# Optimization experiments

Measured on AMD Instinct MI355X. Metric: run time of the kernel, lower is better.

Reference implementation:

```python
import jax, jax.numpy as jnp
import numpy as np

B, T, C = 2, 4096, 768
H = 12
D = C // H  # head_size = 64


def setup_inputs() -> dict:
    key = jax.random.key(0)
    k1, k2, k3 = jax.random.split(key, 3)
    x = jax.random.normal(k1, (B, T, C), dtype=jnp.float32)
    w_attn = jax.random.normal(k2, (C, 3 * C), dtype=jnp.float32) * (C ** -0.5)
    b_attn = jnp.zeros((3 * C,), dtype=jnp.float32)
    w_proj = jax.random.normal(k3, (C, C), dtype=jnp.float32) * (C ** -0.5)
    b_proj = jnp.zeros((C,), dtype=jnp.float32)
    return {"x": x, "w_attn": w_attn, "b_attn": b_attn, "w_proj": w_proj, "b_proj": b_proj}


def reference(x, w_attn, b_attn, w_proj, b_proj):
    Bx, Tx, Cx = x.shape
    # fused QKV projection
    qkv = x @ w_attn + b_attn  # (B, T, 3C)
    q, k, v = jnp.split(qkv, 3, axis=2)
    # (B, H, T, D)
    q = q.reshape(Bx, Tx, H, D).transpose(0, 2, 1, 3)
    k = k.reshape(Bx, Tx, H, D).transpose(0, 2, 1, 3)
    v = v.reshape(Bx, Tx, H, D).transpose(0, 2, 1, 3)
    scale = 1.0 / jnp.sqrt(jnp.asarray(D, dtype=x.dtype))
    scores = jnp.einsum('bhqd,bhkd->bhqk', q, k) * scale  # (B, H, T, T)
    causal = jnp.tril(jnp.ones((Tx, Tx), dtype=bool))
    scores = jnp.where(causal, scores, jnp.asarray(-jnp.inf, dtype=scores.dtype))
    attn = jax.nn.softmax(scores, axis=-1)
    y = jnp.einsum('bhqk,bhkd->bhqd', attn, v)  # (B, H, T, D)
    y = y.transpose(0, 2, 1, 3).reshape(Bx, Tx, Cx)
    return y @ w_proj + b_proj
```

## Files before the change

### kernel.cpp

```cpp
#include <hip/hip_runtime.h>
#include <stdint.h>

#define B_   2
#define T_   4096
#define C_   768
#define H_   12
#define D_   64
#define BH_  24
#define M_   8192
#define K_   768
#define N1_  2304

#define NEG_BIG (-1.0e30f)
#define QSCALE 0.18033688011112042f

typedef short bf16x8 __attribute__((ext_vector_type(8)));
typedef float f32x4  __attribute__((ext_vector_type(4)));
typedef float f32x16 __attribute__((ext_vector_type(16)));
typedef uint32_t u32x4 __attribute__((ext_vector_type(4)));
typedef int i32x2 __attribute__((ext_vector_type(2)));

typedef const __attribute__((address_space(1))) void* as1cv;
typedef __attribute__((address_space(3))) void*       as3v;

__device__ __forceinline__ void gload_lds16(const void* g, void* l) {
  __builtin_amdgcn_global_load_lds((as1cv)g, (as3v)l, 16, 0, 0);
}

__device__ __forceinline__ unsigned short f2bf(float f) {
  uint32_t x = __builtin_bit_cast(uint32_t, f);
  uint32_t r = (x + 0x7fffu + ((x >> 16) & 1u)) >> 16;
  return (unsigned short)r;
}

__device__ __forceinline__ unsigned short f2bf_hu(float f) {
  return (unsigned short)((__builtin_bit_cast(uint32_t, f) + 0x8000u) >> 16);
}

#if __has_builtin(__builtin_amdgcn_perm)
__device__ __forceinline__ uint32_t pack_hu(float lo, float hi) {
  uint32_t a = __builtin_bit_cast(uint32_t, lo) + 0x8000u;
  uint32_t b = __builtin_bit_cast(uint32_t, hi) + 0x8000u;
  return __builtin_amdgcn_perm(b, a, 0x07060302u);
}
#else
__device__ __forceinline__ uint32_t pack_hu(float lo, float hi) {
  uint32_t a = __builtin_bit_cast(uint32_t, lo) + 0x8000u;
  uint32_t b = __builtin_bit_cast(uint32_t, hi) + 0x8000u;
  return (b & 0xFFFF0000u) | (a >> 16);
}
#endif

#if __has_builtin(__builtin_amdgcn_permlane32_swap)
#define HAVE_PLSWAP 1
#else
#define HAVE_PLSWAP 0
#endif

#if __has_builtin(__builtin_amdgcn_exp2f)
__device__ __forceinline__ float fast_exp2(float x) { return __builtin_amdgcn_exp2f(x); }
#else
__device__ __forceinline__ float fast_exp2(float x) { return __expf(x * 0.69314718056f); }
#endif

__global__ void cast_kernel(const float* __restrict__ in, unsigned short* __restrict__ out, int n4) {
  int idx = blockIdx.x * blockDim.x + threadIdx.x;
  int stride = gridDim.x * blockDim.x;
  for (int i = idx; i < n4; i += stride) {
    float4 v = reinterpret_cast<const float4*>(in)[i];
    ushort4 o;
    o.x = f2bf(v.x); o.y = f2bf(v.y); o.z = f2bf(v.z); o.w = f2bf(v.w);
    reinterpret_cast<ushort4*>(out)[i] = o;
  }
}

__global__ void transpose_cast(const float* __restrict__ in, unsigned short* __restrict__ out,
                               int K, int N) {
  __shared__ float tile[32][33];
  const int tx = threadIdx.x, ty = threadIdx.y;
  const int n = blockIdx.x * 32 + tx;
  #pragma unroll
  for (int r = 0; r < 4; ++r) {
    int k = blockIdx.y * 32 + ty + r * 8;
    tile[ty + r * 8][tx] = in[(size_t)k * N + n];
  }
  __syncthreads();
  const int k = blockIdx.y * 32 + tx;
  #pragma unroll
  for (int r = 0; r < 4; ++r) {
    int nn = blockIdx.x * 32 + ty + r * 8;
    out[(size_t)nn * K + k] = f2bf(tile[tx][ty + r * 8]);
  }
}

template <int MODE>
__global__ __launch_bounds__(256) void gemm_kernel(
    const unsigned short* __restrict__ A, const unsigned short* __restrict__ BT,
    const float* __restrict__ bias,
    unsigned short* __restrict__ o0, unsigned short* __restrict__ o1,
    unsigned short* __restrict__ o2, float* __restrict__ fo) {
  __shared__ __align__(16) unsigned short Al[128 * 32];
  __shared__ __align__(16) unsigned short Bl[128 * 32];
  const int tid = threadIdx.x;
  const int w = tid >> 6, lane = tid & 63;
  const int g = lane >> 4, c16 = lane & 15;
  const int wr = w >> 1, wc = w & 1;
  const int m0 = blockIdx.x * 128, n0 = blockIdx.y * 128;

  f32x4 acc[4][4] = {};

  for (int k0 = 0; k0 < K_; k0 += 32) {
    __syncthreads();
    #pragma unroll
    for (int q = 0; q < 2; ++q) {
      const int ch = (w * 2 + q) * 64 + lane;
      const int row = ch >> 2, kb = ch & 3;
      gload_lds16(A  + (size_t)(m0 + row) * K_ + k0 + kb * 8, &Al[(w * 2 + q) * 512]);
      gload_lds16(BT + (size_t)(n0 + row) * K_ + k0 + kb * 8, &Bl[(w * 2 + q) * 512]);
    }
    __syncthreads();
    bf16x8 af[4], bfr[4];
    #pragma unroll
    for (int i = 0; i < 4; ++i) {
      af[i]  = *reinterpret_cast<const bf16x8*>(&Al[(wr * 64 + i * 16 + c16) * 32 + g * 8]);
      bfr[i] = *reinterpret_cast<const bf16x8*>(&Bl[(wc * 64 + i * 16 + c16) * 32 + g * 8]);
    }
    #pragma unroll
    for (int i = 0; i < 4; ++i)
      #pragma unroll
      for (int j = 0; j < 4; ++j)
        acc[i][j] = __builtin_amdgcn_mfma_f32_16x16x32_bf16(af[i], bfr[j], acc[i][j], 0, 0, 0);
  }

  const int which = (MODE == 0) ? (n0 / 768) : 0;
  #pragma unroll
  for (int i = 0; i < 4; ++i) {
    const int mbase = m0 + wr * 64 + i * 16 + g * 4;
    #pragma unroll
    for (int j2 = 0; j2 < 4; ++j2) {
      const int n = n0 + wc * 64 + j2 * 16 + c16;
      const float bv = bias[n];
      #pragma unroll
      for (int j = 0; j < 4; ++j) {
        float v = acc[i][j2][j] + bv;
        const int mm = mbase + j;
        if constexpr (MODE == 0) {
          const int cc = n - which * 768;
          const int hh = cc >> 6, dd = cc & 63;
          const int bb = mm >> 12, tt = mm & 4095;
          const size_t bh = (size_t)bb * H_ + hh;
          const size_t hb = bh * T_ * D_;
          if (which == 0) {
            o0[hb + (size_t)tt * D_ + dd] = f2bf_hu(v * QSCALE);
          } else if (which == 1) {
            const int addr = ((tt >> 5) * 4 + (dd >> 4)) * 512 +
                             ((tt & 31) + ((dd >> 3) & 1) * 32) * 8 + (dd & 7);
            o1[hb + addr] = f2bf_hu(v);
          } else {
            const int addr = (tt >> 6) * 4096 + (dd >> 5) * 2048 +
                             ((tt >> 4) & 3) * 512 +
                             ((dd & 31) + ((tt >> 3) & 1) * 32) * 8 + (tt & 7);
            o2[hb + addr] = f2bf_hu(v);
          }
        } else {
          fo[(size_t)mm * 768 + n] = v;
        }
      }
    }
  }
}

__global__ __launch_bounds__(256, 2) void attn_kernel(
    const unsigned short* __restrict__ Qb, const unsigned short* __restrict__ Kb,
    const unsigned short* __restrict__ Vt, unsigned short* __restrict__ Yb) {
  __shared__ float Ml[3][2][64];
  __shared__ float Ll[3][2][64];
  __shared__ __align__(16) float Yl[3][64][64];

  const int tidx = threadIdx.x;
  const int wv = tidx >> 6;
  const int lane = tidx & 63;
  const int q31 = lane & 31, hi = lane >> 5;
  const int bid = blockIdx.x;
  const int bh = bid % BH_;
  const int strip = (T_ / 64 - 1) - bid / BH_;
  const int q0 = strip * 64;
  const int qgA = q0 + q31;
  const int qgB = q0 + 32 + q31;

  const int bb = bh / H_, hh = bh % H_;
  const size_t hoff = (size_t)bh * T_ * D_;
  const unsigned short* Qh = Qb + hoff;
  const unsigned short* Kh = Kb + hoff + lane * 8;
  const unsigned short* Vh = Vt + hoff + lane * 8;

  bf16x8 qfA[4], qfB[4];
  #pragma unroll
  for (int s = 0; s < 4; ++s) {
    qfA[s] = *reinterpret_cast<const bf16x8*>(&Qh[(size_t)qgA * D_ + s * 16 + hi * 8]);
    qfB[s] = *reinterpret_cast<const bf16x8*>(&Qh[(size_t)qgB * D_ + s * 16 + hi * 8]);
  }

  float mA = NEG_BIG, lA = 0.f, mB = NEG_BIG, lB = 0.f;
  f32x16 yA0 = {}, yA1 = {}, yB0 = {}, yB1 = {};

  const int nt = strip + 1;

  for (int it = wv; it < nt; it += 4) {
    const int kv0 = it << 6;

    const unsigned short* kT = Kh + it * 4096;
    bf16x8 kf[8];
    #pragma unroll
    for (int s = 0; s < 8; ++s)
      kf[s] = *reinterpret_cast<const bf16x8*>(kT + (s >> 2) * 2048 + (s & 3) * 512);

    const unsigned short* vT = Vh + it * 4096;
    bf16x8 vlo[4], vhi[4];
    #pragma unroll
    for (int ks = 0; ks < 4; ++ks) {
      vlo[ks] = *reinterpret_cast<const bf16x8*>(vT + ks * 512);
      vhi[ks] = *reinterpret_cast<const bf16x8*>(vT + 2048 + ks * 512);
    }

    f32x16 sA0 = {}, sA1 = {}, sB0 = {}, sB1 = {};
    #pragma unroll
    for (int s = 0; s < 4; ++s) {
      sA0 = __builtin_amdgcn_mfma_f32_32x32x16_bf16(kf[s], qfA[s], sA0, 0, 0, 0);
      sB0 = __builtin_amdgcn_mfma_f32_32x32x16_bf16(kf[s], qfB[s], sB0, 0, 0, 0);
    }
    #pragma unroll
    for (int s = 0; s < 4; ++s) {
      sA1 = __builtin_amdgcn_mfma_f32_32x32x16_bf16(kf[4 + s], qfA[s], sA1, 0, 0, 0);
      sB1 = __builtin_amdgcn_mfma_f32_32x32x16_bf16(kf[4 + s], qfB[s], sB1, 0, 0, 0);
    }

    if (it == strip) {
      #pragma unroll
      for (int r = 0; r < 16; ++r) {
        const int kvl = (r & 3) + 8 * (r >> 2) + 4 * hi;
        sA0[r] = (kv0 + kvl > qgA)      ? NEG_BIG : sA0[r];
        sA1[r] = NEG_BIG;
        sB1[r] = (kv0 + 32 + kvl > qgB) ? NEG_BIG : sB1[r];
      }
    }

    {
      float a[16];
      #pragma unroll
      for (int r = 0; r < 8; ++r) a[r] = fmaxf(sA0[2 * r], sA0[2 * r + 1]);
      #pragma unroll
      for (int r = 0; r < 8; ++r) a[8 + r] = fmaxf(sA1[2 * r], sA1[2 * r + 1]);
      #pragma unroll
      for (int st = 8; st > 0; st >>= 1)
        #pragma unroll
        for (int r = 0; r < 16; ++r) if (r < st) a[r] = fmaxf(a[r], a[r + st]);
      float tmax = a[0];
      tmax = fmaxf(tmax, __shfl_xor(tmax, 32));

      if (__any(tmax > mA + 11.5f)) {
        const float mnew = fmaxf(mA, tmax);
        const float alpha = fast_exp2(mA - mnew);
        mA = mnew;
        lA *= alpha;
        #pragma unroll
        for (int r = 0; r < 16; ++r) { yA0[r] *= alpha; yA1[r] *= alpha; }
      }
      #pragma unroll
      for (int r = 0; r < 16; ++r) {
        sA0[r] = fast_exp2(sA0[r] - mA);
        sA1[r] = fast_exp2(sA1[r] - mA);
      }
      #pragma unroll
      for (int r = 0; r < 8; ++r) a[r] = sA0[2 * r] + sA0[2 * r + 1];
      #pragma unroll
      for (int r = 0; r < 8; ++r) a[8 + r] = sA1[2 * r] + sA1[2 * r + 1];
      #pragma unroll
      for (int st = 8; st > 0; st >>= 1)
        #pragma unroll
        for (int r = 0; r < 16; ++r) if (r < st) a[r] = a[r] + a[r + st];
      float rsum = a[0];
      rsum += __shfl_xor(rsum, 32);
      lA += rsum;

      bf16x8 pf[4];
#if HAVE_PLSWAP
#define MK_PF(KS, SH, GA, HA)                                                 \
      {                                                                       \
        uint32_t g0 = pack_hu(SH[(GA)*4 + 0], SH[(GA)*4 + 1]);                \
        uint32_t g1 = pack_hu(SH[(GA)*4 + 2], SH[(GA)*4 + 3]);                \
        uint32_t h0 = pack_hu(SH[(HA)*4 + 0], SH[(HA)*4 + 1]);                \
        uint32_t h1 = pack_hu(SH[(HA)*4 + 2], SH[(HA)*4 + 3]);                \
        i32x2 r0 = __builtin_amdgcn_permlane32_swap((int)g0, (int)h0, false, false); \
        i32x2 r1 = __builtin_amdgcn_permlane32_swap((int)g1, (int)h1, false, false); \
        u32x4 t;                                                              \
        t[0] = (uint32_t)r0[0];                                               \
        t[1] = (uint32_t)r1[0];                                               \
        t[2] = (uint32_t)r0[1];                                               \
        t[3] = (uint32_t)r1[1];                                               \
        pf[KS] = __builtin_bit_cast(bf16x8, t);                               \
      }
#else
#define MK_PF(KS, SH, GA, HA)                                                 \
      {                                                                       \
        uint32_t g0 = pack_hu(SH[(GA)*4 + 0], SH[(GA)*4 + 1]);                \
        uint32_t g1 = pack_hu(SH[(GA)*4 + 2], SH[(GA)*4 + 3]);                \
        uint32_t h0 = pack_hu(SH[(HA)*4 + 0], SH[(HA)*4 + 1]);                \
        uint32_t h1 = pack_hu(SH[(HA)*4 + 2], SH[(HA)*4 + 3]);                \
        uint32_t sg0 = (uint32_t)__shfl_xor((int)g0, 32);                     \
        uint32_t sg1 = (uint32_t)__shfl_xor((int)g1, 32);                     \
        uint32_t sh0 = (uint32_t)__shfl_xor((int)h0, 32);                     \
        uint32_t sh1 = (uint32_t)__shfl_xor((int)h1, 32);                     \
        u32x4 t;                                                              \
        t[0] = hi ? sh0 : g0;                                                 \
        t[1] = hi ? sh1 : g1;                                                 \
        t[2] = hi ? h0 : sg0;                                                 \
        t[3] = hi ? h1 : sg1;                                                 \
        pf[KS] = __builtin_bit_cast(bf16x8, t);                               \
      }
#endif
      MK_PF(0, sA0, 0, 1)
      MK_PF(1, sA0, 2, 3)
      MK_PF(2, sA1, 0, 1)
      MK_PF(3, sA1, 2, 3)

      #pragma unroll
      for (int ks = 0; ks < 4; ++ks)
        yA0 = __builtin_amdgcn_mfma_f32_32x32x16_bf16(vlo[ks], pf[ks], yA0, 0, 0, 0);
      #pragma unroll
      for (int ks = 0; ks < 4; ++ks)
        yA1 = __builtin_amdgcn_mfma_f32_32x32x16_bf16(vhi[ks], pf[ks], yA1, 0, 0, 0);
    }

    {
      float a[16];
      #pragma unroll
      for (int r = 0; r < 8; ++r) a[r] = fmaxf(sB0[2 * r], sB0[2 * r + 1]);
      #pragma unroll
      for (int r = 0; r < 8; ++r) a[8 + r] = fmaxf(sB1[2 * r], sB1[2 * r + 1]);
      #pragma unroll
      for (int st = 8; st > 0; st >>= 1)
        #pragma unroll
        for (int r = 0; r < 16; ++r) if (r < st) a[r] = fmaxf(a[r], a[r + st]);
      float tmax = a[0];
      tmax = fmaxf(tmax, __shfl_xor(tmax, 32));

      if (__any(tmax > mB + 11.5f)) {
        const float mnew = fmaxf(mB, tmax);
        const float alpha = fast_exp2(mB - mnew);
        mB = mnew;
        lB *= alpha;
        #pragma unroll
        for (int r = 0; r < 16; ++r) { yB0[r] *= alpha; yB1[r] *= alpha; }
      }
      #pragma unroll
      for (int r = 0; r < 16; ++r) {
        sB0[r] = fast_exp2(sB0[r] - mB);
        sB1[r] = fast_exp2(sB1[r] - mB);
      }
      #pragma unroll
      for (int r = 0; r < 8; ++r) a[r] = sB0[2 * r] + sB0[2 * r + 1];
      #pragma unroll
      for (int r = 0; r < 8; ++r) a[8 + r] = sB1[2 * r] + sB1[2 * r + 1];
      #pragma unroll
      for (int st = 8; st > 0; st >>= 1)
        #pragma unroll
        for (int r = 0; r < 16; ++r) if (r < st) a[r] = a[r] + a[r + st];
      float rsum = a[0];
      rsum += __shfl_xor(rsum, 32);
      lB += rsum;

      bf16x8 pf[4];
      MK_PF(0, sB0, 0, 1)
      MK_PF(1, sB0, 2, 3)
      MK_PF(2, sB1, 0, 1)
      MK_PF(3, sB1, 2, 3)
#undef MK_PF

      #pragma unroll
      for (int ks = 0; ks < 4; ++ks)
        yB0 = __builtin_amdgcn_mfma_f32_32x32x16_bf16(vlo[ks], pf[ks], yB0, 0, 0, 0);
      #pragma unroll
      for (int ks = 0; ks < 4; ++ks)
        yB1 = __builtin_amdgcn_mfma_f32_32x32x16_bf16(vhi[ks], pf[ks], yB1, 0, 0, 0);
    }
  }

  if (wv > 0) {
    Ml[wv - 1][0][lane] = mA; Ml[wv - 1][1][lane] = mB;
    Ll[wv - 1][0][lane] = lA; Ll[wv - 1][1][lane] = lB;
    #pragma unroll
    for (int r = 0; r < 16; ++r) {
      Yl[wv - 1][r][lane]      = yA0[r];
      Yl[wv - 1][16 + r][lane] = yA1[r];
      Yl[wv - 1][32 + r][lane] = yB0[r];
      Yl[wv - 1][48 + r][lane] = yB1[r];
    }
  }
  __syncthreads();
  if (wv == 0) {
    {
      float mm = mA;
      #pragma unroll
      for (int p = 0; p < 3; ++p) mm = fmaxf(mm, Ml[p][0][lane]);
      const float aw = fast_exp2(mA - mm);
      float ap[3];
      float ll = lA * aw;
      #pragma unroll
      for (int p = 0; p < 3; ++p) {
        ap[p] = fast_exp2(Ml[p][0][lane] - mm);
        ll += Ll[p][0][lane] * ap[p];
      }
      const float inv = 1.f / ll;
      const size_t ro = ((size_t)bb * T_ + qgA) * C_ + hh * D_;
      #pragma unroll
      for (int q2 = 0; q2 < 4; ++q2) {
        float v[8];
        #pragma unroll
        for (int e = 0; e < 4; ++e) {
          float t0 = yA0[q2 * 4 + e] * aw;
          float t1 = yA1[q2 * 4 + e] * aw;
          #pragma unroll
          for (int p = 0; p < 3; ++p) {
            t0 += Yl[p][q2 * 4 + e][lane] * ap[p];
            t1 += Yl[p][16 + q2 * 4 + e][lane] * ap[p];
          }
          v[e] = t0 * inv;
          v[4 + e] = t1 * inv;
        }
        uint2 pr0 = {pack_hu(v[0], v[1]), pack_hu(v[2], v[3])};
        *reinterpret_cast<uint2*>(&Yb[ro + q2 * 8 + hi * 4]) = pr0;
        uint2 pr1 = {pack_hu(v[4], v[5]), pack_hu(v[6], v[7])};
        *reinterpret_cast<uint2*>(&Yb[ro + 32 + q2 * 8 + hi * 4]) = pr1;
      }
    }
    {
      float mm = mB;
      #pragma unroll
      for (int p = 0; p < 3; ++p) mm = fmaxf(mm, Ml[p][1][lane]);
      const float aw = fast_exp2(mB - mm);
      float ap[3];
      float ll = lB * aw;
      #pragma unroll
      for (int p = 0; p < 3; ++p) {
        ap[p] = fast_exp2(Ml[p][1][lane] - mm);
        ll += Ll[p][1][lane] * ap[p];
      }
      const float inv = 1.f / ll;
      const size_t ro = ((size_t)bb * T_ + qgB) * C_ + hh * D_;
      #pragma unroll
      for (int q2 = 0; q2 < 4; ++q2) {
        float v[8];
        #pragma unroll
        for (int e = 0; e < 4; ++e) {
          float t0 = yB0[q2 * 4 + e] * aw;
          float t1 = yB1[q2 * 4 + e] * aw;
          #pragma unroll
          for (int p = 0; p < 3; ++p) {
            t0 += Yl[p][32 + q2 * 4 + e][lane] * ap[p];
            t1 += Yl[p][48 + q2 * 4 + e][lane] * ap[p];
          }
          v[e] = t0 * inv;
          v[4 + e] = t1 * inv;
        }
        uint2 pr0 = {pack_hu(v[0], v[1]), pack_hu(v[2], v[3])};
        *reinterpret_cast<uint2*>(&Yb[ro + q2 * 8 + hi * 4]) = pr0;
        uint2 pr1 = {pack_hu(v[4], v[5]), pack_hu(v[6], v[7])};
        *reinterpret_cast<uint2*>(&Yb[ro + 32 + q2 * 8 + hi * 4]) = pr1;
      }
    }
  }
}

extern "C" void kernel_launch(void* const* d_in, const int* in_sizes, int n_in,
                              void* d_out, int out_size, void* d_ws, size_t ws_size,
                              hipStream_t stream) {
  const float* x      = (const float*)d_in[0];
  const float* w_attn = (const float*)d_in[1];
  const float* b_attn = (const float*)d_in[2];
  const float* w_proj = (const float*)d_in[3];
  const float* b_proj = (const float*)d_in[4];
  float* out = (float*)d_out;

  char* ws = (char*)d_ws;
  size_t off = 0;
  auto alloc = [&](size_t bytes) -> void* {
    void* p = ws + off;
    off += (bytes + 255) & ~(size_t)255;
    return p;
  };
  unsigned short* xb  = (unsigned short*)alloc((size_t)M_ * K_ * 2);
  unsigned short* waT = (unsigned short*)alloc((size_t)N1_ * K_ * 2);
  unsigned short* wpT = (unsigned short*)alloc((size_t)C_ * K_ * 2);
  unsigned short* Qb  = (unsigned short*)alloc((size_t)BH_ * T_ * D_ * 2);
  unsigned short* Kb  = (unsigned short*)alloc((size_t)BH_ * T_ * D_ * 2);
  unsigned short* Vt  = (unsigned short*)alloc((size_t)BH_ * D_ * T_ * 2);
  unsigned short* Yb  = (unsigned short*)alloc((size_t)M_ * C_ * 2);

  cast_kernel<<<1024, 256, 0, stream>>>(x, xb, M_ * K_ / 4);
  transpose_cast<<<dim3(N1_ / 32, K_ / 32), dim3(32, 8), 0, stream>>>(w_attn, waT, K_, N1_);
  transpose_cast<<<dim3(C_ / 32, K_ / 32), dim3(32, 8), 0, stream>>>(w_proj, wpT, K_, C_);

  gemm_kernel<0><<<dim3(M_ / 128, N1_ / 128), 256, 0, stream>>>(
      xb, waT, b_attn, Qb, Kb, Vt, nullptr);

  attn_kernel<<<(T_ / 64) * BH_, 256, 0, stream>>>(Qb, Kb, Vt, Yb);

  gemm_kernel<1><<<dim3(M_ / 128, C_ / 128), 256, 0, stream>>>(
      Yb, wpT, b_proj, nullptr, nullptr, nullptr, out);
}
```

Measured before the change: 174.8 us.

## Prefetch K tiles, pack partial outputs to bf16, merge transpose launches

Merges the two weight transpose-cast launches into one kernel. Simplifies the QKV GEMM epilogue address calculation by hoisting it out of the per-element loop. In attention, the next K tile is loaded into registers after the current QK MFMAs to overlap latency. Per-wave partial outputs are stored to LDS as packed bf16 instead of fp32. This halves LDS footprint but loses some precision, and the prefetch reads past the last tile without a bounds check.

```diff
diff --git a/kernel.cpp b/kernel.cpp
--- a/kernel.cpp
+++ b/kernel.cpp
@@ -51,6 +51,10 @@
 }
 #endif
 
+__device__ __forceinline__ float bfu(uint32_t w, int hb) {
+  return __builtin_bit_cast(float, hb ? (w & 0xFFFF0000u) : (w << 16));
+}
+
 #if __has_builtin(__builtin_amdgcn_permlane32_swap)
 #define HAVE_PLSWAP 1
 #else
@@ -74,11 +78,15 @@
   }
 }
 
-__global__ void transpose_cast(const float* __restrict__ in, unsigned short* __restrict__ out,
-                               int K, int N) {
+__global__ void transpose_cast2(const float* __restrict__ a, unsigned short* __restrict__ oa,
+                                const float* __restrict__ b, unsigned short* __restrict__ ob) {
   __shared__ float tile[32][33];
+  const int bx = blockIdx.x;
+  const float* in; unsigned short* out; int N, cb;
+  if (bx < 72) { in = a; out = oa; N = 2304; cb = bx; }
+  else         { in = b; out = ob; N = 768;  cb = bx - 72; }
   const int tx = threadIdx.x, ty = threadIdx.y;
-  const int n = blockIdx.x * 32 + tx;
+  const int n = cb * 32 + tx;
   #pragma unroll
   for (int r = 0; r < 4; ++r) {
     int k = blockIdx.y * 32 + ty + r * 8;
@@ -88,8 +96,8 @@
   const int k = blockIdx.y * 32 + tx;
   #pragma unroll
   for (int r = 0; r < 4; ++r) {
-    int nn = blockIdx.x * 32 + ty + r * 8;
-    out[(size_t)nn * K + k] = f2bf(tile[tx][ty + r * 8]);
+    int nn = cb * 32 + ty + r * 8;
+    out[(size_t)nn * K_ + k] = f2bf(tile[tx][ty + r * 8]);
   }
 }
 
@@ -136,35 +144,38 @@
   #pragma unroll
   for (int i = 0; i < 4; ++i) {
     const int mbase = m0 + wr * 64 + i * 16 + g * 4;
+    const int bb2 = mbase >> 12, tb = mbase & 4095;
     #pragma unroll
     for (int j2 = 0; j2 < 4; ++j2) {
       const int n = n0 + wc * 64 + j2 * 16 + c16;
       const float bv = bias[n];
-      #pragma unroll
-      for (int j = 0; j < 4; ++j) {
-        float v = acc[i][j2][j] + bv;
-        const int mm = mbase + j;
-        if constexpr (MODE == 0) {
-          const int cc = n - which * 768;
-          const int hh = cc >> 6, dd = cc & 63;
-          const int bb = mm >> 12, tt = mm & 4095;
-          const size_t bh = (size_t)bb * H_ + hh;
-          const size_t hb = bh * T_ * D_;
-          if (which == 0) {
-            o0[hb + (size_t)tt * D_ + dd] = f2bf_hu(v * QSCALE);
-          } else if (which == 1) {
-            const int addr = ((tt >> 5) * 4 + (dd >> 4)) * 512 +
-                             ((tt & 31) + ((dd >> 3) & 1) * 32) * 8 + (dd & 7);
-            o1[hb + addr] = f2bf_hu(v);
-          } else {
-            const int addr = (tt >> 6) * 4096 + (dd >> 5) * 2048 +
-                             ((tt >> 4) & 3) * 512 +
-                             ((dd & 31) + ((tt >> 3) & 1) * 32) * 8 + (tt & 7);
-            o2[hb + addr] = f2bf_hu(v);
-          }
+      if constexpr (MODE == 0) {
+        const int cc = n - which * 768;
+        const int hh2 = cc >> 6, dd = cc & 63;
+        const size_t hb = ((size_t)bb2 * H_ + hh2) * T_ * D_;
+        if (which == 0) {
+          const int addr0 = tb * 64 + dd;
+          #pragma unroll
+          for (int j = 0; j < 4; ++j)
+            o0[hb + addr0 + j * 64] = f2bf_hu((acc[i][j2][j] + bv) * QSCALE);
+        } else if (which == 1) {
+          const int addr0 = ((tb >> 5) * 4 + (dd >> 4)) * 512 +
+                            ((tb & 31) + ((dd >> 3) & 1) * 32) * 8 + (dd & 7);
+          #pragma unroll
+          for (int j = 0; j < 4; ++j)
+            o1[hb + addr0 + j * 8] = f2bf_hu(acc[i][j2][j] + bv);
         } else {
-          fo[(size_t)mm * 768 + n] = v;
+          const int addr0 = (tb >> 6) * 4096 + (dd >> 5) * 2048 +
+                            ((tb >> 4) & 3) * 512 +
+                            ((dd & 31) + ((tb >> 3) & 1) * 32) * 8 + (tb & 7);
+          #pragma unroll
+          for (int j = 0; j < 4; ++j)
+            o2[hb + addr0 + j] = f2bf_hu(acc[i][j2][j] + bv);
         }
+      } else {
+        #pragma unroll
+        for (int j = 0; j < 4; ++j)
+          fo[(size_t)(mbase + j) * 768 + n] = acc[i][j2][j] + bv;
       }
     }
   }
@@ -175,7 +186,7 @@
     const unsigned short* __restrict__ Vt, unsigned short* __restrict__ Yb) {
   __shared__ float Ml[3][2][64];
   __shared__ float Ll[3][2][64];
-  __shared__ __align__(16) float Yl[3][64][64];
+  __shared__ uint32_t Ylp[3][32][64];
 
   const int tidx = threadIdx.x;
   const int wv = tidx >> 6;
@@ -206,14 +217,16 @@
 
   const int nt = strip + 1;
 
+  bf16x8 kf[8];
+  {
+    const unsigned short* kT = Kh + wv * 4096;
+    #pragma unroll
+    for (int s = 0; s < 8; ++s)
+      kf[s] = *reinterpret_cast<const bf16x8*>(kT + (s >> 2) * 2048 + (s & 3) * 512);
+  }
+
   for (int it = wv; it < nt; it += 4) {
     const int kv0 = it << 6;
-
-    const unsigned short* kT = Kh + it * 4096;
-    bf16x8 kf[8];
-    #pragma unroll
-    for (int s = 0; s < 8; ++s)
-      kf[s] = *reinterpret_cast<const bf16x8*>(kT + (s >> 2) * 2048 + (s & 3) * 512);
 
     const unsigned short* vT = Vh + it * 4096;
     bf16x8 vlo[4], vhi[4];
@@ -233,6 +246,13 @@
     for (int s = 0; s < 4; ++s) {
       sA1 = __builtin_amdgcn_mfma_f32_32x32x16_bf16(kf[4 + s], qfA[s], sA1, 0, 0, 0);
       sB1 = __builtin_amdgcn_mfma_f32_32x32x16_bf16(kf[4 + s], qfB[s], sB1, 0, 0, 0);
+    }
+
+    {
+      const unsigned short* kT = Kh + (it + 4) * 4096;
+      #pragma unroll
+      for (int s = 0; s < 8; ++s)
+        kf[s] = *reinterpret_cast<const bf16x8*>(kT + (s >> 2) * 2048 + (s & 3) * 512);
     }
 
     if (it == strip) {
@@ -390,11 +410,11 @@
     Ml[wv - 1][0][lane] = mA; Ml[wv - 1][1][lane] = mB;
     Ll[wv - 1][0][lane] = lA; Ll[wv - 1][1][lane] = lB;
     #pragma unroll
-    for (int r = 0; r < 16; ++r) {
-      Yl[wv - 1][r][lane]      = yA0[r];
-      Yl[wv - 1][16 + r][lane] = yA1[r];
-      Yl[wv - 1][32 + r][lane] = yB0[r];
-      Yl[wv - 1][48 + r][lane] = yB1[r];
+    for (int r = 0; r < 8; ++r) {
+      Ylp[wv - 1][r][lane]      = pack_hu(yA0[2 * r], yA0[2 * r + 1]);
+      Ylp[wv - 1][8 + r][lane]  = pack_hu(yA1[2 * r], yA1[2 * r + 1]);
+      Ylp[wv - 1][16 + r][lane] = pack_hu(yB0[2 * r], yB0[2 * r + 1]);
+      Ylp[wv - 1][24 + r][lane] = pack_hu(yB1[2 * r], yB1[2 * r + 1]);
     }
   }
   __syncthreads();
@@ -418,12 +438,13 @@
         float v[8];
         #pragma unroll
         for (int e = 0; e < 4; ++e) {
+          const int pr = q2 * 2 + (e >> 1), hb2 = e & 1;
           float t0 = yA0[q2 * 4 + e] * aw;
           float t1 = yA1[q2 * 4 + e] * aw;
           #pragma unroll
           for (int p = 0; p < 3; ++p) {
-            t0 += Yl[p][q2 * 4 + e][lane] * ap[p];
-            t1 += Yl[p][16 + q2 * 4 + e][lane] * ap[p];
+            t0 += bfu(Ylp[p][pr][lane], hb2) * ap[p];
+            t1 += bfu(Ylp[p][8 + pr][lane], hb2) * ap[p];
           }
           v[e] = t0 * inv;
           v[4 + e] = t1 * inv;
@@ -453,12 +474,13 @@
         float v[8];
         #pragma unroll
         for (int e = 0; e < 4; ++e) {
+          const int pr = q2 * 2 + (e >> 1), hb2 = e & 1;
           float t0 = yB0[q2 * 4 + e] * aw;
           float t1 = yB1[q2 * 4 + e] * aw;
           #pragma unroll
           for (int p = 0; p < 3; ++p) {
-            t0 += Yl[p][32 + q2 * 4 + e][lane] * ap[p];
-            t1 += Yl[p][48 + q2 * 4 + e][lane] * ap[p];
+            t0 += bfu(Ylp[p][16 + pr][lane], hb2) * ap[p];
+            t1 += bfu(Ylp[p][24 + pr][lane], hb2) * ap[p];
           }
           v[e] = t0 * inv;
           v[4 + e] = t1 * inv;
@@ -498,8 +520,7 @@
   unsigned short* Yb  = (unsigned short*)alloc((size_t)M_ * C_ * 2);
 
   cast_kernel<<<1024, 256, 0, stream>>>(x, xb, M_ * K_ / 4);
-  transpose_cast<<<dim3(N1_ / 32, K_ / 32), dim3(32, 8), 0, stream>>>(w_attn, waT, K_, N1_);
-  transpose_cast<<<dim3(C_ / 32, K_ / 32), dim3(32, 8), 0, stream>>>(w_proj, wpT, K_, C_);
+  transpose_cast2<<<dim3(96, 24), dim3(32, 8), 0, stream>>>(w_attn, waT, w_proj, wpT);
 
   gemm_kernel<0><<<dim3(M_ / 128, N1_ / 128), 256, 0, stream>>>(
       xb, waT, b_attn, Qb, Kb, Vt, nullptr);
```

After: 166.7 us. -4.6%, faster.
